# Performance work log

Measured on AMD Instinct MI355X. Metric: run time of the kernel, lower is better.

Reference implementation:

```python
import jax, jax.numpy as jnp
import numpy as np

B, N, C_IN = 4, 2048, 256
H, C_HEAD = 8, 32  # c_out=256, concat=True -> 256//8=32 per head
ALPHA = 0.2
NEG_INF = -9e15

def glorot(key, shape, fan_in, fan_out):
    lim = jnp.sqrt(6.0 / (fan_in + fan_out))
    return jax.random.uniform(key, shape, jnp.float32, -lim, lim)

def setup_inputs() -> dict:
    key = jax.random.key(0)
    k1, k2, k3, k4, k5 = jax.random.split(key, 5)
    x = jax.random.normal(k1, (B, N, C_IN), jnp.float32)
    G = jax.random.randint(k2, (B, N, N), 0, 2, jnp.int32)
    # ensure self-loops so no row is fully masked
    eye = jnp.eye(N, dtype=jnp.int32)[None]
    G = jnp.maximum(G, eye)
    proj_kernel = glorot(k3, (C_IN, H * C_HEAD), C_IN, H * C_HEAD)
    proj_bias = jnp.zeros((H * C_HEAD,), jnp.float32)
    attn_fst = glorot(k4, (H, C_HEAD), H, C_HEAD)
    attn_snd = glorot(k5, (H, C_HEAD), H, C_HEAD)
    return {"x": x, "G": G, "proj_kernel": proj_kernel, "proj_bias": proj_bias,
            "attn_fst": attn_fst, "attn_snd": attn_snd}

def reference(x, G, proj_kernel, proj_bias, attn_fst, attn_snd):
    b, n = x.shape[0], x.shape[1]
    h = (x @ proj_kernel + proj_bias).reshape(b, n, H, C_HEAD)  # [B,N,H,c]
    lf = jnp.einsum('bnhc,hc->bnh', h, attn_fst)  # [B,N,H]
    ls = jnp.einsum('bnhc,hc->bnh', h, attn_snd)  # [B,N,H]
    logit = lf[:, :, None, :] + ls[:, None, :, :]  # [B,N,N,H]
    logit = jax.nn.leaky_relu(logit, negative_slope=ALPHA)
    logit = jnp.where(G[..., None] == 1, logit, NEG_INF)
    attn = jax.nn.softmax(logit, axis=2)
    out = jnp.einsum('bijh,bjhc->bihc', attn, h)  # [B,N,H,c]
    return out.reshape(b, n, H * C_HEAD)  # concat=True
```

## Files before the change

### kernel.cpp

```cpp
#include <hip/hip_runtime.h>

#define BB 4
#define NN 2048
#define CIN 256
#define HH 8
#define COUT 256
#define LOG2E 1.44269504088896340736f

#define PBM 128
#define PBN 64
#define PKT 16
#define NKT (CIN / PKT)
#define TI 8
#define CJ 64
#define NC (NN / CJ)

__global__ __launch_bounds__(256) void gat_proj(
    const float* __restrict__ x, const float* __restrict__ W,
    const float* __restrict__ bias, const float* __restrict__ afst,
    const float* __restrict__ asnd, float* __restrict__ hout,
    float* __restrict__ lfT, float* __restrict__ lsT)
{
    __shared__ float xsT[2][PKT][PBM + 4];
    __shared__ float wls[2][PKT][PBN + 4];
    const int t = threadIdx.x;
    const int bx = blockIdx.x & 3;
    const int by = blockIdx.x >> 2;
    const int row0 = by * PBM, col0 = bx * PBN;
    const int tx = t & 15, ty = t >> 4;

    const int srow = t >> 2;
    const int skq  = (t & 3) * 4;
    const float* xb0 = x + (size_t)(row0 + srow) * CIN + skq;
    const float* xb1 = x + (size_t)(row0 + 64 + srow) * CIN + skq;
    const int swk = t >> 4, swc = (t & 15) * 4;
    const float* wb = W + (size_t)swk * COUT + col0 + swc;

    float4 xr0 = *(const float4*)xb0;
    float4 xr1 = *(const float4*)xb1;
    float4 wr  = *(const float4*)wb;
    xsT[0][skq+0][srow] = xr0.x; xsT[0][skq+1][srow] = xr0.y;
    xsT[0][skq+2][srow] = xr0.z; xsT[0][skq+3][srow] = xr0.w;
    xsT[0][skq+0][64+srow] = xr1.x; xsT[0][skq+1][64+srow] = xr1.y;
    xsT[0][skq+2][64+srow] = xr1.z; xsT[0][skq+3][64+srow] = xr1.w;
    *(float4*)&wls[0][swk][swc] = wr;
    __syncthreads();

    float acc[8][4];
#pragma unroll
    for (int i = 0; i < 8; ++i)
#pragma unroll
        for (int j = 0; j < 4; ++j) acc[i][j] = 0.f;

    for (int kt = 0; kt < NKT; ++kt) {
        if (kt + 1 < NKT) {
            xr0 = *(const float4*)(xb0 + (kt + 1) * PKT);
            xr1 = *(const float4*)(xb1 + (kt + 1) * PKT);
            wr  = *(const float4*)(wb + (size_t)(kt + 1) * PKT * COUT);
        }
        const int cur = kt & 1;
#pragma unroll
        for (int k = 0; k < PKT; ++k) {
            float xv[8], wv[4];
            *(float4*)&xv[0] = *(const float4*)&xsT[cur][k][ty * 8];
            *(float4*)&xv[4] = *(const float4*)&xsT[cur][k][ty * 8 + 4];
            *(float4*)&wv[0] = *(const float4*)&wls[cur][k][tx * 4];
#pragma unroll
            for (int i = 0; i < 8; ++i)
#pragma unroll
                for (int j = 0; j < 4; ++j)
                    acc[i][j] = fmaf(xv[i], wv[j], acc[i][j]);
        }
        __syncthreads();
        if (kt + 1 < NKT) {
            const int nxt = cur ^ 1;
            xsT[nxt][skq+0][srow] = xr0.x; xsT[nxt][skq+1][srow] = xr0.y;
            xsT[nxt][skq+2][srow] = xr0.z; xsT[nxt][skq+3][srow] = xr0.w;
            xsT[nxt][skq+0][64+srow] = xr1.x; xsT[nxt][skq+1][64+srow] = xr1.y;
            xsT[nxt][skq+2][64+srow] = xr1.z; xsT[nxt][skq+3][64+srow] = xr1.w;
            *(float4*)&wls[nxt][swk][swc] = wr;
            __syncthreads();
        }
    }

    const float4 bv = *(const float4*)(bias + col0 + tx * 4);
    const float4 af = *(const float4*)(afst + col0 + tx * 4);
    const float4 as = *(const float4*)(asnd + col0 + tx * 4);
    const int hd = (col0 + tx * 4) >> 5;
#pragma unroll
    for (int i = 0; i < 8; ++i) {
        float4 o;
        o.x = acc[i][0] + bv.x; o.y = acc[i][1] + bv.y;
        o.z = acc[i][2] + bv.z; o.w = acc[i][3] + bv.w;
        const int row = row0 + ty * 8 + i;
        *(float4*)(hout + (size_t)row * COUT + col0 + tx * 4) = o;
        float pf = o.x * af.x + o.y * af.y + o.z * af.z + o.w * af.w;
        float ps = o.x * as.x + o.y * as.y + o.z * as.z + o.w * as.w;
#pragma unroll
        for (int off = 1; off < 8; off <<= 1) {
            pf += __shfl_xor(pf, off);
            ps += __shfl_xor(ps, off);
        }
        if ((tx & 7) == 0) {
            const int b = row >> 11, n = row & (NN - 1);
            lfT[(size_t)(b * HH + hd) * NN + n] = pf * LOG2E;
            lsT[(size_t)(b * HH + hd) * NN + n] = ps * LOG2E;
        }
    }
}

__device__ __forceinline__ int eoff4(int jl, int h, int half) {
    return jl * 64 + ((((h << 1) + half) ^ (jl & 7)) << 2);
}

__global__ __launch_bounds__(256) void gat_attn(
    const int* __restrict__ G, const float* __restrict__ hin,
    const float* __restrict__ lfT, const float* __restrict__ lsT,
    float* __restrict__ out)
{
    __shared__ __align__(16) float e_lds[CJ * 64];
    __shared__ unsigned g_lds[4][CJ];
    __shared__ float s_lds[TI][HH];

    const int t = threadIdx.x;
    const int b = blockIdx.x >> 8;
    const int i0 = (blockIdx.x & 255) * TI;
    const int h = t >> 5, jj = t & 31;
    const int w = t >> 6, l = t & 63;
    const int hh = l >> 3;

    const float* lsrow = lsT + (size_t)(b * HH + h) * NN;
    float lfv[TI];
#pragma unroll
    for (int r = 0; r < TI; ++r)
        lfv[r] = lfT[(size_t)(b * HH + h) * NN + i0 + r];

    float sp[TI], a[TI][4];
#pragma unroll
    for (int r = 0; r < TI; ++r) {
        sp[r] = 0.f;
#pragma unroll
        for (int c2 = 0; c2 < 4; ++c2) a[r][c2] = 0.f;
    }

    const int* gbase = G + ((size_t)b * NN + i0 + 2 * w) * NN + l;
    int g0 = gbase[0], g1 = gbase[NN];
    float ls0 = lsrow[jj], ls1 = lsrow[32 + jj];

    for (int c = 0; c < NC; ++c) {
        const int j0 = c * CJ;
        g_lds[w][l] = (g0 ? 1u : 0u) | (g1 ? 2u : 0u);
        __syncthreads();
        {
            const unsigned gmA = g_lds[0][jj] | (g_lds[1][jj] << 2) |
                                 (g_lds[2][jj] << 4) | (g_lds[3][jj] << 6);
            const unsigned gmB = g_lds[0][jj+32] | (g_lds[1][jj+32] << 2) |
                                 (g_lds[2][jj+32] << 4) | (g_lds[3][jj+32] << 6);
            float ev[TI];
#pragma unroll
            for (int r = 0; r < TI; ++r) {
                float s = lfv[r] + ls0;
                s = fmaxf(s, 0.2f * s);
                ev[r] = ((gmA >> r) & 1u) ? exp2f(s) : 0.f;
                sp[r] += ev[r];
            }
            *(float4*)&e_lds[eoff4(jj, h, 0)] = make_float4(ev[0], ev[1], ev[2], ev[3]);
            *(float4*)&e_lds[eoff4(jj, h, 1)] = make_float4(ev[4], ev[5], ev[6], ev[7]);
#pragma unroll
            for (int r = 0; r < TI; ++r) {
                float s = lfv[r] + ls1;
                s = fmaxf(s, 0.2f * s);
                ev[r] = ((gmB >> r) & 1u) ? exp2f(s) : 0.f;
                sp[r] += ev[r];
            }
            *(float4*)&e_lds[eoff4(jj+32, h, 0)] = make_float4(ev[0], ev[1], ev[2], ev[3]);
            *(float4*)&e_lds[eoff4(jj+32, h, 1)] = make_float4(ev[4], ev[5], ev[6], ev[7]);
        }
        __syncthreads();
        if (c + 1 < NC) {
            const int* gp = gbase + (size_t)(j0 + CJ);
            g0 = gp[0]; g1 = gp[NN];
            ls0 = lsrow[j0 + CJ + jj]; ls1 = lsrow[j0 + CJ + 32 + jj];
        }
        {
            const float* hbase = hin + ((size_t)b * NN + j0) * COUT + (l << 2);
            float4 hq[4];
#pragma unroll
            for (int p = 0; p < 4; ++p)
                hq[p] = *(const float4*)(hbase + (size_t)(w + p * 4) * COUT);
#pragma unroll
            for (int it = 0; it < CJ / 4; ++it) {
                const int jl = w + it * 4;
                const float4 hv = hq[it & 3];
                if (it + 4 < CJ / 4)
                    hq[it & 3] = *(const float4*)(hbase + (size_t)(jl + 16) * COUT);
                const float4 lo = *(const float4*)&e_lds[eoff4(jl, hh, 0)];
                const float4 hi = *(const float4*)&e_lds[eoff4(jl, hh, 1)];
                const float ee[8] = {lo.x, lo.y, lo.z, lo.w, hi.x, hi.y, hi.z, hi.w};
                const float hvv[4] = {hv.x, hv.y, hv.z, hv.w};
#pragma unroll
                for (int r = 0; r < TI; ++r)
#pragma unroll
                    for (int c2 = 0; c2 < 4; ++c2)
                        a[r][c2] = fmaf(ee[r], hvv[c2], a[r][c2]);
            }
        }
        __syncthreads();
    }
#pragma unroll
    for (int off = 16; off; off >>= 1) {
#pragma unroll
        for (int r = 0; r < TI; ++r) sp[r] += __shfl_xor(sp[r], off);
    }
    if (jj == 0) {
#pragma unroll
        for (int r = 0; r < TI; ++r) s_lds[r][h] = sp[r];
    }
    float* buf = e_lds;
    if (w >= 2) {
#pragma unroll
        for (int r = 0; r < TI; ++r)
#pragma unroll
            for (int c2 = 0; c2 < 4; ++c2)
                buf[((w - 2) << 11) + ((r * 4 + c2) << 6) + l] = a[r][c2];
    }
    __syncthreads();
    if (w < 2) {
#pragma unroll
        for (int r = 0; r < TI; ++r)
#pragma unroll
            for (int c2 = 0; c2 < 4; ++c2)
                a[r][c2] += buf[(w << 11) + ((r * 4 + c2) << 6) + l];
    }
    __syncthreads();
    if (w == 1) {
#pragma unroll
        for (int r = 0; r < TI; ++r)
#pragma unroll
            for (int c2 = 0; c2 < 4; ++c2)
                buf[((r * 4 + c2) << 6) + l] = a[r][c2];
    }
    __syncthreads();
    if (w == 0) {
#pragma unroll
        for (int r = 0; r < TI; ++r) {
            const float inv = 1.f / s_lds[r][hh];
            float4 o;
            o.x = (a[r][0] + buf[((r * 4 + 0) << 6) + l]) * inv;
            o.y = (a[r][1] + buf[((r * 4 + 1) << 6) + l]) * inv;
            o.z = (a[r][2] + buf[((r * 4 + 2) << 6) + l]) * inv;
            o.w = (a[r][3] + buf[((r * 4 + 3) << 6) + l]) * inv;
            *(float4*)(out + (size_t)(b * NN + i0 + r) * COUT + (l << 2)) = o;
        }
    }
}

extern "C" void kernel_launch(void* const* d_in, const int* in_sizes, int n_in,
                              void* d_out, int out_size, void* d_ws, size_t ws_size,
                              hipStream_t stream) {
    const float* x    = (const float*)d_in[0];
    const int*   G    = (const int*)d_in[1];
    const float* W    = (const float*)d_in[2];
    const float* bias = (const float*)d_in[3];
    const float* afst = (const float*)d_in[4];
    const float* asnd = (const float*)d_in[5];
    float* out = (float*)d_out;

    float* h_ws   = (float*)d_ws;
    float* lfT_ws = h_ws + (size_t)BB * NN * COUT;
    float* lsT_ws = lfT_ws + (size_t)BB * HH * NN;

    hipLaunchKernelGGL(gat_proj, dim3((BB * NN / PBM) * (COUT / PBN)), dim3(256),
                       0, stream, x, W, bias, afst, asnd, h_ws, lfT_ws, lsT_ws);
    hipLaunchKernelGGL(gat_attn, dim3(BB * (NN / TI)), dim3(256), 0, stream,
                       G, h_ws, lfT_ws, lsT_ws, out);
}
```

Baseline: 285.4 us.

## Retile attention PV accumulation to 8x8 per thread and widen projection blocks

The attention kernel's PV loop now has each thread accumulate 8 rows by 8 channels. Each wave splits the 64-node chunk into two interleaved halves that are combined with a cross-half shuffle before the existing cross-wave LDS reduction. This raises FMA work per h load and per LDS read of the exp weights, at the cost of more accumulator registers. The projection GEMM moves to 512-thread blocks with a 4x4 micro-tile per thread, trading per-thread reuse for more threads in flight.

```diff
diff --git a/kernel.cpp b/kernel.cpp
--- a/kernel.cpp
+++ b/kernel.cpp
@@ -15,7 +15,7 @@
 #define CJ 64
 #define NC (NN / CJ)
 
-__global__ __launch_bounds__(256) void gat_proj(
+__global__ __launch_bounds__(512) void gat_proj(
     const float* __restrict__ x, const float* __restrict__ W,
     const float* __restrict__ bias, const float* __restrict__ afst,
     const float* __restrict__ asnd, float* __restrict__ hout,
@@ -29,56 +29,50 @@
     const int row0 = by * PBM, col0 = bx * PBN;
     const int tx = t & 15, ty = t >> 4;
 
-    const int srow = t >> 2;
-    const int skq  = (t & 3) * 4;
-    const float* xb0 = x + (size_t)(row0 + srow) * CIN + skq;
-    const float* xb1 = x + (size_t)(row0 + 64 + srow) * CIN + skq;
+    const int srow = t >> 2, skq = (t & 3) * 4;
+    const float* xb = x + (size_t)(row0 + srow) * CIN + skq;
     const int swk = t >> 4, swc = (t & 15) * 4;
     const float* wb = W + (size_t)swk * COUT + col0 + swc;
 
-    float4 xr0 = *(const float4*)xb0;
-    float4 xr1 = *(const float4*)xb1;
-    float4 wr  = *(const float4*)wb;
-    xsT[0][skq+0][srow] = xr0.x; xsT[0][skq+1][srow] = xr0.y;
-    xsT[0][skq+2][srow] = xr0.z; xsT[0][skq+3][srow] = xr0.w;
-    xsT[0][skq+0][64+srow] = xr1.x; xsT[0][skq+1][64+srow] = xr1.y;
-    xsT[0][skq+2][64+srow] = xr1.z; xsT[0][skq+3][64+srow] = xr1.w;
-    *(float4*)&wls[0][swk][swc] = wr;
-    __syncthreads();
-
-    float acc[8][4];
-#pragma unroll
-    for (int i = 0; i < 8; ++i)
+    float4 xr = *(const float4*)xb;
+    float4 wr;
+    if (t < 256) wr = *(const float4*)wb;
+    xsT[0][skq+0][srow] = xr.x; xsT[0][skq+1][srow] = xr.y;
+    xsT[0][skq+2][srow] = xr.z; xsT[0][skq+3][srow] = xr.w;
+    if (t < 256) *(float4*)&wls[0][swk][swc] = wr;
+    __syncthreads();
+
+    float acc[4][4];
+#pragma unroll
+    for (int i = 0; i < 4; ++i)
 #pragma unroll
         for (int j = 0; j < 4; ++j) acc[i][j] = 0.f;
 
     for (int kt = 0; kt < NKT; ++kt) {
         if (kt + 1 < NKT) {
-            xr0 = *(const float4*)(xb0 + (kt + 1) * PKT);
-            xr1 = *(const float4*)(xb1 + (kt + 1) * PKT);
-            wr  = *(const float4*)(wb + (size_t)(kt + 1) * PKT * COUT);
+            xr = *(const float4*)(xb + (kt + 1) * PKT);
+            if (t < 256) wr = *(const float4*)(wb + (size_t)(kt + 1) * PKT * COUT);
         }
         const int cur = kt & 1;
 #pragma unroll
         for (int k = 0; k < PKT; ++k) {
-            float xv[8], wv[4];
-            *(float4*)&xv[0] = *(const float4*)&xsT[cur][k][ty * 8];
-            *(float4*)&xv[4] = *(const float4*)&xsT[cur][k][ty * 8 + 4];
-            *(float4*)&wv[0] = *(const float4*)&wls[cur][k][tx * 4];
-#pragma unroll
-            for (int i = 0; i < 8; ++i)
-#pragma unroll
-                for (int j = 0; j < 4; ++j)
-                    acc[i][j] = fmaf(xv[i], wv[j], acc[i][j]);
+            const float4 xv = *(const float4*)&xsT[cur][k][ty * 4];
+            const float4 wv = *(const float4*)&wls[cur][k][tx * 4];
+            acc[0][0]=fmaf(xv.x,wv.x,acc[0][0]); acc[0][1]=fmaf(xv.x,wv.y,acc[0][1]);
+            acc[0][2]=fmaf(xv.x,wv.z,acc[0][2]); acc[0][3]=fmaf(xv.x,wv.w,acc[0][3]);
+            acc[1][0]=fmaf(xv.y,wv.x,acc[1][0]); acc[1][1]=fmaf(xv.y,wv.y,acc[1][1]);
+            acc[1][2]=fmaf(xv.y,wv.z,acc[1][2]); acc[1][3]=fmaf(xv.y,wv.w,acc[1][3]);
+            acc[2][0]=fmaf(xv.z,wv.x,acc[2][0]); acc[2][1]=fmaf(xv.z,wv.y,acc[2][1]);
+            acc[2][2]=fmaf(xv.z,wv.z,acc[2][2]); acc[2][3]=fmaf(xv.z,wv.w,acc[2][3]);
+            acc[3][0]=fmaf(xv.w,wv.x,acc[3][0]); acc[3][1]=fmaf(xv.w,wv.y,acc[3][1]);
+            acc[3][2]=fmaf(xv.w,wv.z,acc[3][2]); acc[3][3]=fmaf(xv.w,wv.w,acc[3][3]);
         }
         __syncthreads();
         if (kt + 1 < NKT) {
             const int nxt = cur ^ 1;
-            xsT[nxt][skq+0][srow] = xr0.x; xsT[nxt][skq+1][srow] = xr0.y;
-            xsT[nxt][skq+2][srow] = xr0.z; xsT[nxt][skq+3][srow] = xr0.w;
-            xsT[nxt][skq+0][64+srow] = xr1.x; xsT[nxt][skq+1][64+srow] = xr1.y;
-            xsT[nxt][skq+2][64+srow] = xr1.z; xsT[nxt][skq+3][64+srow] = xr1.w;
-            *(float4*)&wls[nxt][swk][swc] = wr;
+            xsT[nxt][skq+0][srow] = xr.x; xsT[nxt][skq+1][srow] = xr.y;
+            xsT[nxt][skq+2][srow] = xr.z; xsT[nxt][skq+3][srow] = xr.w;
+            if (t < 256) *(float4*)&wls[nxt][swk][swc] = wr;
             __syncthreads();
         }
     }
@@ -88,19 +82,17 @@
     const float4 as = *(const float4*)(asnd + col0 + tx * 4);
     const int hd = (col0 + tx * 4) >> 5;
 #pragma unroll
-    for (int i = 0; i < 8; ++i) {
+    for (int i = 0; i < 4; ++i) {
         float4 o;
         o.x = acc[i][0] + bv.x; o.y = acc[i][1] + bv.y;
         o.z = acc[i][2] + bv.z; o.w = acc[i][3] + bv.w;
-        const int row = row0 + ty * 8 + i;
+        const int row = row0 + ty * 4 + i;
         *(float4*)(hout + (size_t)row * COUT + col0 + tx * 4) = o;
         float pf = o.x * af.x + o.y * af.y + o.z * af.z + o.w * af.w;
         float ps = o.x * as.x + o.y * as.y + o.z * as.z + o.w * as.w;
-#pragma unroll
-        for (int off = 1; off < 8; off <<= 1) {
-            pf += __shfl_xor(pf, off);
-            ps += __shfl_xor(ps, off);
-        }
+        pf += __shfl_xor(pf, 1); ps += __shfl_xor(ps, 1);
+        pf += __shfl_xor(pf, 2); ps += __shfl_xor(ps, 2);
+        pf += __shfl_xor(pf, 4); ps += __shfl_xor(ps, 4);
         if ((tx & 7) == 0) {
             const int b = row >> 11, n = row & (NN - 1);
             lfT[(size_t)(b * HH + hd) * NN + n] = pf * LOG2E;
@@ -127,7 +119,9 @@
     const int i0 = (blockIdx.x & 255) * TI;
     const int h = t >> 5, jj = t & 31;
     const int w = t >> 6, l = t & 63;
-    const int hh = l >> 3;
+    const int l5 = l >> 5;
+    const int ph = (l >> 2) & 7;
+    const int ch0 = ph * 32 + (l & 3) * 8;
 
     const float* lsrow = lsT + (size_t)(b * HH + h) * NN;
     float lfv[TI];
@@ -135,12 +129,13 @@
     for (int r = 0; r < TI; ++r)
         lfv[r] = lfT[(size_t)(b * HH + h) * NN + i0 + r];
 
-    float sp[TI], a[TI][4];
-#pragma unroll
-    for (int r = 0; r < TI; ++r) {
+    float sp[TI];
+    float a[8][8];
+#pragma unroll
+    for (int r = 0; r < 8; ++r) {
         sp[r] = 0.f;
 #pragma unroll
-        for (int c2 = 0; c2 < 4; ++c2) a[r][c2] = 0.f;
+        for (int cc = 0; cc < 8; ++cc) a[r][cc] = 0.f;
     }
 
     const int* gbase = G + ((size_t)b * NN + i0 + 2 * w) * NN + l;
@@ -183,26 +178,28 @@
             ls0 = lsrow[j0 + CJ + jj]; ls1 = lsrow[j0 + CJ + 32 + jj];
         }
         {
-            const float* hbase = hin + ((size_t)b * NN + j0) * COUT + (l << 2);
-            float4 hq[4];
-#pragma unroll
-            for (int p = 0; p < 4; ++p)
-                hq[p] = *(const float4*)(hbase + (size_t)(w + p * 4) * COUT);
-#pragma unroll
-            for (int it = 0; it < CJ / 4; ++it) {
-                const int jl = w + it * 4;
-                const float4 hv = hq[it & 3];
-                if (it + 4 < CJ / 4)
-                    hq[it & 3] = *(const float4*)(hbase + (size_t)(jl + 16) * COUT);
-                const float4 lo = *(const float4*)&e_lds[eoff4(jl, hh, 0)];
-                const float4 hi = *(const float4*)&e_lds[eoff4(jl, hh, 1)];
-                const float ee[8] = {lo.x, lo.y, lo.z, lo.w, hi.x, hi.y, hi.z, hi.w};
-                const float hvv[4] = {hv.x, hv.y, hv.z, hv.w};
-#pragma unroll
-                for (int r = 0; r < TI; ++r)
-#pragma unroll
-                    for (int c2 = 0; c2 < 4; ++c2)
-                        a[r][c2] = fmaf(ee[r], hvv[c2], a[r][c2]);
+            const float* hb = hin + ((size_t)b * NN + j0 + w + 4 * l5) * COUT + ch0;
+            float4 hA = *(const float4*)hb;
+            float4 hB = *(const float4*)(hb + 4);
+#pragma unroll
+            for (int p = 0; p < 8; ++p) {
+                const int jl = w + 8 * p + 4 * l5;
+                const float4 lo = *(const float4*)&e_lds[eoff4(jl, ph, 0)];
+                const float4 hi = *(const float4*)&e_lds[eoff4(jl, ph, 1)];
+                float4 hA2, hB2;
+                if (p < 7) {
+                    hA2 = *(const float4*)(hb + (size_t)(p + 1) * 8 * COUT);
+                    hB2 = *(const float4*)(hb + (size_t)(p + 1) * 8 * COUT + 4);
+                }
+#define PV8(ER, EV) \
+    a[ER][0]=fmaf(EV,hA.x,a[ER][0]); a[ER][1]=fmaf(EV,hA.y,a[ER][1]); \
+    a[ER][2]=fmaf(EV,hA.z,a[ER][2]); a[ER][3]=fmaf(EV,hA.w,a[ER][3]); \
+    a[ER][4]=fmaf(EV,hB.x,a[ER][4]); a[ER][5]=fmaf(EV,hB.y,a[ER][5]); \
+    a[ER][6]=fmaf(EV,hB.z,a[ER][6]); a[ER][7]=fmaf(EV,hB.w,a[ER][7]);
+                PV8(0, lo.x) PV8(1, lo.y) PV8(2, lo.z) PV8(3, lo.w)
+                PV8(4, hi.x) PV8(5, hi.y) PV8(6, hi.z) PV8(7, hi.w)
+#undef PV8
+                hA = hA2; hB = hB2;
             }
         }
         __syncthreads();
@@ -216,41 +213,52 @@
 #pragma unroll
         for (int r = 0; r < TI; ++r) s_lds[r][h] = sp[r];
     }
+#pragma unroll
+    for (int r = 0; r < 8; ++r)
+#pragma unroll
+        for (int cc = 0; cc < 8; ++cc)
+            a[r][cc] += __shfl_xor(a[r][cc], 32);
     float* buf = e_lds;
-    if (w >= 2) {
-#pragma unroll
-        for (int r = 0; r < TI; ++r)
-#pragma unroll
-            for (int c2 = 0; c2 < 4; ++c2)
-                buf[((w - 2) << 11) + ((r * 4 + c2) << 6) + l] = a[r][c2];
-    }
-    __syncthreads();
-    if (w < 2) {
-#pragma unroll
-        for (int r = 0; r < TI; ++r)
-#pragma unroll
-            for (int c2 = 0; c2 < 4; ++c2)
-                a[r][c2] += buf[(w << 11) + ((r * 4 + c2) << 6) + l];
-    }
-    __syncthreads();
-    if (w == 1) {
-#pragma unroll
-        for (int r = 0; r < TI; ++r)
-#pragma unroll
-            for (int c2 = 0; c2 < 4; ++c2)
-                buf[((r * 4 + c2) << 6) + l] = a[r][c2];
-    }
-    __syncthreads();
-    if (w == 0) {
-#pragma unroll
-        for (int r = 0; r < TI; ++r) {
-            const float inv = 1.f / s_lds[r][hh];
-            float4 o;
-            o.x = (a[r][0] + buf[((r * 4 + 0) << 6) + l]) * inv;
-            o.y = (a[r][1] + buf[((r * 4 + 1) << 6) + l]) * inv;
-            o.z = (a[r][2] + buf[((r * 4 + 2) << 6) + l]) * inv;
-            o.w = (a[r][3] + buf[((r * 4 + 3) << 6) + l]) * inv;
-            *(float4*)(out + (size_t)(b * NN + i0 + r) * COUT + (l << 2)) = o;
+    if (w >= 2 && l < 32) {
+#pragma unroll
+        for (int r = 0; r < 8; ++r)
+#pragma unroll
+            for (int cc = 0; cc < 8; ++cc)
+                buf[((w - 2) << 11) + ((r * 8 + cc) << 5) + l] = a[r][cc];
+    }
+    __syncthreads();
+    if (w < 2 && l < 32) {
+#pragma unroll
+        for (int r = 0; r < 8; ++r)
+#pragma unroll
+            for (int cc = 0; cc < 8; ++cc)
+                a[r][cc] += buf[(w << 11) + ((r * 8 + cc) << 5) + l];
+    }
+    __syncthreads();
+    if (w == 1 && l < 32) {
+#pragma unroll
+        for (int r = 0; r < 8; ++r)
+#pragma unroll
+            for (int cc = 0; cc < 8; ++cc)
+                buf[((r * 8 + cc) << 5) + l] = a[r][cc];
+    }
+    __syncthreads();
+    if (w == 0 && l < 32) {
+#pragma unroll
+        for (int r = 0; r < 8; ++r) {
+            const float inv = 1.f / s_lds[r][ph];
+            float4 o1, o2;
+            o1.x = (a[r][0] + buf[((r * 8 + 0) << 5) + l]) * inv;
+            o1.y = (a[r][1] + buf[((r * 8 + 1) << 5) + l]) * inv;
+            o1.z = (a[r][2] + buf[((r * 8 + 2) << 5) + l]) * inv;
+            o1.w = (a[r][3] + buf[((r * 8 + 3) << 5) + l]) * inv;
+            o2.x = (a[r][4] + buf[((r * 8 + 4) << 5) + l]) * inv;
+            o2.y = (a[r][5] + buf[((r * 8 + 5) << 5) + l]) * inv;
+            o2.z = (a[r][6] + buf[((r * 8 + 6) << 5) + l]) * inv;
+            o2.w = (a[r][7] + buf[((r * 8 + 7) << 5) + l]) * inv;
+            float* op = out + (size_t)(b * NN + i0 + r) * COUT + ch0;
+            *(float4*)op = o1;
+            *(float4*)(op + 4) = o2;
         }
     }
 }
@@ -270,7 +278,7 @@
     float* lfT_ws = h_ws + (size_t)BB * NN * COUT;
     float* lsT_ws = lfT_ws + (size_t)BB * HH * NN;
 
-    hipLaunchKernelGGL(gat_proj, dim3((BB * NN / PBM) * (COUT / PBN)), dim3(256),
+    hipLaunchKernelGGL(gat_proj, dim3((BB * NN / PBM) * (COUT / PBN)), dim3(512),
                        0, stream, x, W, bias, afst, asnd, h_ws, lfT_ws, lsT_ws);
     hipLaunchKernelGGL(gat_attn, dim3(BB * (NN / TI)), dim3(256), 0, stream,
                        G, h_ws, lfT_ws, lsT_ws, out);
```

Measured after the change: 293.5 us. 1.03x slower.
